# Optimization experiments

Measured on AMD Instinct MI355X. Metric: run time of the kernel, lower is better.

Reference implementation:

```python
import jax, jax.numpy as jnp
import numpy as np


def setup_inputs() -> dict:
    key = jax.random.key(0)
    ks = jax.random.split(key, 8)
    N, E, D, MAX_NODES, C = 100000, 1536, 128, 250000, 2
    embeddings = jax.random.normal(ks[0], (N, E), dtype=jnp.float32)
    node_ids = jnp.arange(N, dtype=jnp.int64)  # default global_ids path
    # persistent node memory buffer (warm state mid-sequence)
    memory = jax.random.normal(ks[1], (MAX_NODES, D), dtype=jnp.float32) * 0.1
    s_ih = 1.0 / np.sqrt(E)
    s_hh = 1.0 / np.sqrt(D)
    w_ih = jax.random.normal(ks[2], (3 * D, E), dtype=jnp.float32) * s_ih
    w_hh = jax.random.normal(ks[3], (3 * D, D), dtype=jnp.float32) * s_hh
    b_ih = jax.random.normal(ks[4], (3 * D,), dtype=jnp.float32) * s_hh
    b_hh = jax.random.normal(ks[5], (3 * D,), dtype=jnp.float32) * s_hh
    s_c = 1.0 / np.sqrt(E + D)
    cls_w = jax.random.normal(ks[6], (C, E + D), dtype=jnp.float32) * s_c
    cls_b = jax.random.normal(ks[7], (C,), dtype=jnp.float32) * s_c
    return {"embeddings": embeddings, "node_ids": node_ids, "memory": memory,
            "w_ih": w_ih, "w_hh": w_hh, "b_ih": b_ih, "b_hh": b_hh,
            "cls_w": cls_w, "cls_b": cls_b}


def reference(embeddings, node_ids, memory, w_ih, w_hh, b_ih, b_hh, cls_w, cls_b):
    # gather previous memory rows for the active nodes: [N, D]
    prev = memory[node_ids]
    # torch.nn.GRUCell math
    gi = embeddings @ w_ih.T + b_ih  # [N, 3D]
    gh = prev @ w_hh.T + b_hh        # [N, 3D]
    i_r, i_z, i_n = jnp.split(gi, 3, axis=1)
    h_r, h_z, h_n = jnp.split(gh, 3, axis=1)
    r = jax.nn.sigmoid(i_r + h_r)
    z = jax.nn.sigmoid(i_z + h_z)
    n = jnp.tanh(i_n + r * h_n)
    new_mem = (1.0 - z) * n + z * prev  # [N, D]
    # scatter updated rows back into the persistent buffer (detached in torch)
    updated_memory = memory.at[node_ids].set(jax.lax.stop_gradient(new_mem))
    # classifier on [embeddings ; new_mem]; dropout is identity in eval
    combined = jnp.concatenate([embeddings, new_mem], axis=1)
    logits = combined @ cls_w.T + cls_b  # [N, 2]
    return logits, updated_memory
```

## Files before the change

### kernel.cpp

```cpp
#include <hip/hip_runtime.h>
#include <hip/hip_bf16.h>

typedef __bf16 bf16;
typedef __bf16 bf16x4 __attribute__((ext_vector_type(4)));
typedef __bf16 bf16x8 __attribute__((ext_vector_type(8)));
typedef float  f32x4  __attribute__((ext_vector_type(4)));

#define EDIM 1536
#define DDIM 128
#define CDIM 1664
#define TM   64
#define NCH  48

#define MFMA_B16(a, b, c) __builtin_amdgcn_mfma_f32_16x16x32_bf16((a), (b), (c), 0, 0, 0)

__device__ __forceinline__ float sigf(float x) { return 1.0f / (1.0f + __expf(-x)); }
__device__ __forceinline__ float tanhf_fast(float x) { return 2.0f / (1.0f + __expf(-2.0f * x)) - 1.0f; }

__device__ __forceinline__ void glds16(const void* g, void* l) {
  __builtin_amdgcn_global_load_lds(
      (const __attribute__((address_space(1))) unsigned int*)g,
      (__attribute__((address_space(3))) unsigned int*)l, 16, 0, 0);
}

template <int LDA>
__device__ __forceinline__ void stageW(const bf16* __restrict__ w, int k0,
                                       char* dst, int wave, int lane) {
#pragma unroll
  for (int j = 0; j < 3; ++j) {
    const int segbase = j * 512 + wave * 64;
    const int seg = segbase + lane;
    const int n = seg >> 2;
    const int q = seg & 3;
    glds16(w + (size_t)n * LDA + k0 + q * 8, dst + (size_t)segbase * 16);
  }
}

__global__ __launch_bounds__(256) void prep_convert(const float* __restrict__ w_ih,
                                                    const float* __restrict__ w_hh,
                                                    bf16* __restrict__ wib,
                                                    bf16* __restrict__ whb) {
  const int i = (blockIdx.x * 256 + threadIdx.x) * 4;
  const int TIH = 3 * DDIM * EDIM;
  const int THH = 3 * DDIM * DDIM;
  if (i < TIH) {
    const float4 v = *(const float4*)(w_ih + i);
    bf16x4 o = {(bf16)v.x, (bf16)v.y, (bf16)v.z, (bf16)v.w};
    *(bf16x4*)(wib + i) = o;
  } else if (i < TIH + THH) {
    const int j = i - TIH;
    const float4 v = *(const float4*)(w_hh + j);
    bf16x4 o = {(bf16)v.x, (bf16)v.y, (bf16)v.z, (bf16)v.w};
    *(bf16x4*)(whb + j) = o;
  }
}

__global__ __launch_bounds__(512, 4) void gru_fused(
    const float* __restrict__ emb, const int* __restrict__ ids,
    const float* __restrict__ mem,
    const float* __restrict__ b_ih, const float* __restrict__ b_hh,
    const float* __restrict__ cls_w, const float* __restrict__ cls_b,
    const bf16* __restrict__ wib, const bf16* __restrict__ whb,
    float* __restrict__ logits, float* __restrict__ omem, int Nrows)
{
  __shared__ char  sW[2][24576];
  __shared__ char  sA[2][5120];
  __shared__ char  sP[16384];
  __shared__ float sLp[64][2];
  __shared__ int   sIds[64];

  const int t    = threadIdx.x;
  const int lane = t & 63;
  const int wave = t >> 6;
  const int wm   = wave >> 2;
  const int wn   = wave & 3;
  const int l15  = lane & 15;
  const int lq   = lane >> 4;
  const int m0   = blockIdx.x * TM;

  if (t < 64)  sIds[t] = (m0 + t < Nrows) ? ids[m0 + t] : 0;
  if (t < 128) sLp[t >> 1][t & 1] = cls_b[t & 1];

  f32x4 accR[2][2], accZ[2][2], accN[2][2], accH[2][2];
#pragma unroll
  for (int sub = 0; sub < 2; ++sub) {
    const int nc = wn * 32 + sub * 16 + l15;
    const float br = b_ih[nc] + b_hh[nc];
    const float bz = b_ih[128 + nc] + b_hh[128 + nc];
    const float bn = b_ih[256 + nc];
    const float bh = b_hh[256 + nc];
#pragma unroll
    for (int mt = 0; mt < 2; ++mt) {
      accR[mt][sub] = (f32x4){br, br, br, br};
      accZ[mt][sub] = (f32x4){bz, bz, bz, bz};
      accN[mt][sub] = (f32x4){bn, bn, bn, bn};
      accH[mt][sub] = (f32x4){bh, bh, bh, bh};
    }
  }

  const int  ar = t >> 3;
  const int  aq = t & 7;
  const bool av = (m0 + ar) < Nrows;
  const float* pA = emb + (size_t)(m0 + ar) * EDIM + aq * 4;
  const int  awofs = ar * 80 + aq * 8;
  float lp0 = 0.f, lp1 = 0.f;

  stageW<EDIM>(wib, 0, sW[0], wave, lane);
  {
    float4 a = make_float4(0.f, 0.f, 0.f, 0.f);
    if (av) a = *(const float4*)pA;
    const float4 c0 = *(const float4*)(cls_w + aq * 4);
    const float4 c1 = *(const float4*)(cls_w + CDIM + aq * 4);
    lp0 += a.x * c0.x + a.y * c0.y + a.z * c0.z + a.w * c0.w;
    lp1 += a.x * c1.x + a.y * c1.y + a.z * c1.z + a.w * c1.w;
    bf16x4 o = {(bf16)a.x, (bf16)a.y, (bf16)a.z, (bf16)a.w};
    *(bf16x4*)(sA[0] + awofs) = o;
  }
  __syncthreads();

  for (int s = 0; s < NCH; ++s) {
    const int cur = s & 1, nxt = cur ^ 1;
    const bool pf = (s + 1) < NCH;
    if (pf) stageW<EDIM>(wib, (s + 1) * 32, sW[nxt], wave, lane);

    bf16x8 af[2];
#pragma unroll
    for (int mt = 0; mt < 2; ++mt) {
      const int m = wm * 32 + mt * 16 + l15;
      af[mt] = *(bf16x8*)(sA[cur] + m * 80 + lq * 16);
    }
#pragma unroll
    for (int g = 0; g < 3; ++g) {
#pragma unroll
      for (int sub = 0; sub < 2; ++sub) {
        const int n = g * 128 + wn * 32 + sub * 16 + l15;
        const bf16x8 bfr = *(bf16x8*)(sW[cur] + n * 64 + lq * 16);
        if (g == 0) {
          accR[0][sub] = MFMA_B16(af[0], bfr, accR[0][sub]);
          accR[1][sub] = MFMA_B16(af[1], bfr, accR[1][sub]);
        } else if (g == 1) {
          accZ[0][sub] = MFMA_B16(af[0], bfr, accZ[0][sub]);
          accZ[1][sub] = MFMA_B16(af[1], bfr, accZ[1][sub]);
        } else {
          accN[0][sub] = MFMA_B16(af[0], bfr, accN[0][sub]);
          accN[1][sub] = MFMA_B16(af[1], bfr, accN[1][sub]);
        }
      }
    }
    if (pf) {
      const int kn = (s + 1) * 32;
      float4 a = make_float4(0.f, 0.f, 0.f, 0.f);
      if (av) a = *(const float4*)(pA + kn);
      const float4 c0 = *(const float4*)(cls_w + kn + aq * 4);
      const float4 c1 = *(const float4*)(cls_w + CDIM + kn + aq * 4);
      lp0 += a.x * c0.x + a.y * c0.y + a.z * c0.z + a.w * c0.w;
      lp1 += a.x * c1.x + a.y * c1.y + a.z * c1.z + a.w * c1.w;
      bf16x4 o = {(bf16)a.x, (bf16)a.y, (bf16)a.z, (bf16)a.w};
      *(bf16x4*)(sA[nxt] + awofs) = o;
    }
    __syncthreads();
  }

  {
    float v0 = lp0, v1 = lp1;
    v0 += __shfl_xor(v0, 1); v0 += __shfl_xor(v0, 2); v0 += __shfl_xor(v0, 4);
    v1 += __shfl_xor(v1, 1); v1 += __shfl_xor(v1, 2); v1 += __shfl_xor(v1, 4);
    if ((lane & 7) == 0) {
      atomicAdd(&sLp[ar][0], v0);
      atomicAdd(&sLp[ar][1], v1);
    }
  }

  stageW<DDIM>(whb, 0, sW[0], wave, lane);
  {
    const int prow = t >> 5;
    const int pc   = t & 31;
#pragma unroll
    for (int p = 0; p < 4; ++p) {
      const int r = p * 16 + prow;
      const float4 v = *(const float4*)(mem + (size_t)sIds[r] * DDIM + pc * 4);
      bf16x4 o = {(bf16)v.x, (bf16)v.y, (bf16)v.z, (bf16)v.w};
      *(bf16x4*)(sP + r * 256 + ((pc << 3) ^ ((r & 7) << 4))) = o;
    }
  }
  __syncthreads();

  for (int ks = 0; ks < 4; ++ks) {
    const int cur = ks & 1, nxt = cur ^ 1;
    if (ks + 1 < 4) stageW<DDIM>(whb, (ks + 1) * 32, sW[nxt], wave, lane);
    bf16x8 af[2];
#pragma unroll
    for (int mt = 0; mt < 2; ++mt) {
      const int m = wm * 32 + mt * 16 + l15;
      const int kb = (ks * 32 + lq * 8) << 1;
      af[mt] = *(bf16x8*)(sP + m * 256 + (kb ^ ((m & 7) << 4)));
    }
#pragma unroll
    for (int g = 0; g < 3; ++g) {
#pragma unroll
      for (int sub = 0; sub < 2; ++sub) {
        const int n = g * 128 + wn * 32 + sub * 16 + l15;
        const bf16x8 bfr = *(bf16x8*)(sW[cur] + n * 64 + lq * 16);
        if (g == 0) {
          accR[0][sub] = MFMA_B16(af[0], bfr, accR[0][sub]);
          accR[1][sub] = MFMA_B16(af[1], bfr, accR[1][sub]);
        } else if (g == 1) {
          accZ[0][sub] = MFMA_B16(af[0], bfr, accZ[0][sub]);
          accZ[1][sub] = MFMA_B16(af[1], bfr, accZ[1][sub]);
        } else {
          accH[0][sub] = MFMA_B16(af[0], bfr, accH[0][sub]);
          accH[1][sub] = MFMA_B16(af[1], bfr, accH[1][sub]);
        }
      }
    }
    __syncthreads();
  }

  float lpM[8][2];
#pragma unroll
  for (int i = 0; i < 8; ++i) { lpM[i][0] = 0.f; lpM[i][1] = 0.f; }

#pragma unroll
  for (int mt = 0; mt < 2; ++mt) {
#pragma unroll
    for (int sub = 0; sub < 2; ++sub) {
      const int d = wn * 32 + sub * 16 + l15;
      const float cw0 = cls_w[EDIM + d];
      const float cw1 = cls_w[CDIM + EDIM + d];
#pragma unroll
      for (int j = 0; j < 4; ++j) {
        const int m = wm * 32 + mt * 16 + lq * 4 + j;
        const float r = sigf(accR[mt][sub][j]);
        const float z = sigf(accZ[mt][sub][j]);
        const float n = tanhf_fast(accN[mt][sub][j] + r * accH[mt][sub][j]);
        const float pv = mem[(size_t)sIds[m] * DDIM + d];
        const float nv = (1.0f - z) * n + z * pv;
        if (m0 + m < Nrows) omem[(size_t)sIds[m] * DDIM + d] = nv;
        lpM[mt * 4 + j][0] += nv * cw0;
        lpM[mt * 4 + j][1] += nv * cw1;
      }
    }
  }

#pragma unroll
  for (int i = 0; i < 8; ++i) {
#pragma unroll
    for (int c = 0; c < 2; ++c) {
      float v = lpM[i][c];
      v += __shfl_xor(v, 1); v += __shfl_xor(v, 2);
      v += __shfl_xor(v, 4); v += __shfl_xor(v, 8);
      if (l15 == 0) {
        const int m = wm * 32 + (i >> 2) * 16 + lq * 4 + (i & 3);
        atomicAdd(&sLp[m][c], v);
      }
    }
  }
  __syncthreads();

  if (t < 128) {
    const int m = t >> 1, c = t & 1;
    if (m0 + m < Nrows) logits[(size_t)(m0 + m) * 2 + c] = sLp[m][c];
  }
}

extern "C" void kernel_launch(void* const* d_in, const int* in_sizes, int n_in,
                              void* d_out, int out_size, void* d_ws, size_t ws_size,
                              hipStream_t stream) {
  const float* emb   = (const float*)d_in[0];
  const int*   ids   = (const int*)d_in[1];
  const float* mem   = (const float*)d_in[2];
  const float* w_ih  = (const float*)d_in[3];
  const float* w_hh  = (const float*)d_in[4];
  const float* b_ih  = (const float*)d_in[5];
  const float* b_hh  = (const float*)d_in[6];
  const float* cls_w = (const float*)d_in[7];
  const float* cls_b = (const float*)d_in[8];

  const int N    = in_sizes[0] / EDIM;
  const int MAXN = in_sizes[2] / DDIM;

  float* logits = (float*)d_out;
  float* omem   = (float*)d_out + (size_t)N * 2;
  bf16*  wib    = (bf16*)d_ws;
  bf16*  whb    = wib + 3 * DDIM * EDIM;

  hipMemcpyAsync(omem, mem, (size_t)MAXN * DDIM * sizeof(float),
                 hipMemcpyDeviceToDevice, stream);
  const int prep_threads = (3 * DDIM * EDIM + 3 * DDIM * DDIM) / 4;
  prep_convert<<<(prep_threads + 255) / 256, 256, 0, stream>>>(w_ih, w_hh, wib, whb);
  gru_fused<<<(N + TM - 1) / TM, 512, 0, stream>>>(emb, ids, mem, b_ih, b_hh,
                                                   cls_w, cls_b, wib, whb,
                                                   logits, omem, N);
}
```

Measured before the change: 421.5 us.

## Load GRU weight fragments directly into registers and halve row tile

Weight tiles no longer go through shared memory. Each wave now loads its bf16 weight fragments straight from global memory into registers, double-buffered across K steps through an unrolled two-stage macro. The row tile shrinks from 64 to 32 and the block from 512 to 256 threads, so there are twice as many blocks and less shared memory per block. This removes the LDS staging traffic and the shared-memory footprint, but each block now rereads the full weight matrix from global/L2 for only 32 rows, which doubles total weight traffic and adds register pressure.

```diff
diff --git a/kernel.cpp b/kernel.cpp
--- a/kernel.cpp
+++ b/kernel.cpp
@@ -9,32 +9,13 @@
 #define EDIM 1536
 #define DDIM 128
 #define CDIM 1664
-#define TM   64
-#define NCH  48
+#define TM   32
+#define NSTG 48
 
 #define MFMA_B16(a, b, c) __builtin_amdgcn_mfma_f32_16x16x32_bf16((a), (b), (c), 0, 0, 0)
 
 __device__ __forceinline__ float sigf(float x) { return 1.0f / (1.0f + __expf(-x)); }
 __device__ __forceinline__ float tanhf_fast(float x) { return 2.0f / (1.0f + __expf(-2.0f * x)) - 1.0f; }
-
-__device__ __forceinline__ void glds16(const void* g, void* l) {
-  __builtin_amdgcn_global_load_lds(
-      (const __attribute__((address_space(1))) unsigned int*)g,
-      (__attribute__((address_space(3))) unsigned int*)l, 16, 0, 0);
-}
-
-template <int LDA>
-__device__ __forceinline__ void stageW(const bf16* __restrict__ w, int k0,
-                                       char* dst, int wave, int lane) {
-#pragma unroll
-  for (int j = 0; j < 3; ++j) {
-    const int segbase = j * 512 + wave * 64;
-    const int seg = segbase + lane;
-    const int n = seg >> 2;
-    const int q = seg & 3;
-    glds16(w + (size_t)n * LDA + k0 + q * 8, dst + (size_t)segbase * 16);
-  }
-}
 
 __global__ __launch_bounds__(256) void prep_convert(const float* __restrict__ w_ih,
                                                     const float* __restrict__ w_hh,
@@ -55,7 +36,7 @@
   }
 }
 
-__global__ __launch_bounds__(512, 4) void gru_fused(
+__global__ __launch_bounds__(256, 2) void gru_fused(
     const float* __restrict__ emb, const int* __restrict__ ids,
     const float* __restrict__ mem,
     const float* __restrict__ b_ih, const float* __restrict__ b_hh,
@@ -63,23 +44,20 @@
     const bf16* __restrict__ wib, const bf16* __restrict__ whb,
     float* __restrict__ logits, float* __restrict__ omem, int Nrows)
 {
-  __shared__ char  sW[2][24576];
-  __shared__ char  sA[2][5120];
-  __shared__ char  sP[16384];
-  __shared__ float sLp[64][2];
-  __shared__ int   sIds[64];
+  __shared__ char  sA[2][2560];
+  __shared__ char  sP[8192];
+  __shared__ float sLp[32][2];
+  __shared__ int   sIds[32];
 
   const int t    = threadIdx.x;
   const int lane = t & 63;
-  const int wave = t >> 6;
-  const int wm   = wave >> 2;
-  const int wn   = wave & 3;
+  const int wn   = t >> 6;
   const int l15  = lane & 15;
   const int lq   = lane >> 4;
   const int m0   = blockIdx.x * TM;
 
-  if (t < 64)  sIds[t] = (m0 + t < Nrows) ? ids[m0 + t] : 0;
-  if (t < 128) sLp[t >> 1][t & 1] = cls_b[t & 1];
+  if (t < 32) sIds[t] = (m0 + t < Nrows) ? ids[m0 + t] : 0;
+  if (t < 64) sLp[t >> 1][t & 1] = cls_b[t & 1];
 
   f32x4 accR[2][2], accZ[2][2], accN[2][2], accH[2][2];
 #pragma unroll
@@ -105,7 +83,52 @@
   const int  awofs = ar * 80 + aq * 8;
   float lp0 = 0.f, lp1 = 0.f;
 
-  stageW<EDIM>(wib, 0, sW[0], wave, lane);
+  const bf16* pW = wib + (size_t)(wn * 32 + l15) * EDIM + lq * 8;
+
+  bf16x8 wP[6], wQ[6];
+
+#define LOADW(DST, S) do {                                    \
+    const bf16* _p = pW + (size_t)(S) * 32;                   \
+    DST[0] = *(const bf16x8*)(_p);                            \
+    DST[1] = *(const bf16x8*)(_p +  16 * EDIM);               \
+    DST[2] = *(const bf16x8*)(_p + 128 * EDIM);               \
+    DST[3] = *(const bf16x8*)(_p + 144 * EDIM);               \
+    DST[4] = *(const bf16x8*)(_p + 256 * EDIM);               \
+    DST[5] = *(const bf16x8*)(_p + 272 * EDIM);               \
+  } while (0)
+
+#define BODY(S, CUR, WC, WNX, PF) do {                                        \
+    float4 a = make_float4(0.f, 0.f, 0.f, 0.f), c0 = a, c1 = a;               \
+    if (PF) {                                                                 \
+      LOADW(WNX, (S) + 1);                                                    \
+      if (av) a = *(const float4*)(pA + ((S) + 1) * 32);                      \
+      c0 = *(const float4*)(cls_w + ((S) + 1) * 32 + aq * 4);                 \
+      c1 = *(const float4*)(cls_w + CDIM + ((S) + 1) * 32 + aq * 4);          \
+    }                                                                         \
+    bf16x8 af0 = *(bf16x8*)(sA[CUR] + (l15) * 80 + lq * 16);                  \
+    bf16x8 af1 = *(bf16x8*)(sA[CUR] + (16 + l15) * 80 + lq * 16);             \
+    accR[0][0] = MFMA_B16(af0, WC[0], accR[0][0]);                            \
+    accR[1][0] = MFMA_B16(af1, WC[0], accR[1][0]);                            \
+    accR[0][1] = MFMA_B16(af0, WC[1], accR[0][1]);                            \
+    accR[1][1] = MFMA_B16(af1, WC[1], accR[1][1]);                            \
+    accZ[0][0] = MFMA_B16(af0, WC[2], accZ[0][0]);                            \
+    accZ[1][0] = MFMA_B16(af1, WC[2], accZ[1][0]);                            \
+    accZ[0][1] = MFMA_B16(af0, WC[3], accZ[0][1]);                            \
+    accZ[1][1] = MFMA_B16(af1, WC[3], accZ[1][1]);                            \
+    accN[0][0] = MFMA_B16(af0, WC[4], accN[0][0]);                            \
+    accN[1][0] = MFMA_B16(af1, WC[4], accN[1][0]);                            \
+    accN[0][1] = MFMA_B16(af0, WC[5], accN[0][1]);                            \
+    accN[1][1] = MFMA_B16(af1, WC[5], accN[1][1]);                            \
+    if (PF) {                                                                 \
+      lp0 += a.x * c0.x + a.y * c0.y + a.z * c0.z + a.w * c0.w;               \
+      lp1 += a.x * c1.x + a.y * c1.y + a.z * c1.z + a.w * c1.w;               \
+      bf16x4 o = {(bf16)a.x, (bf16)a.y, (bf16)a.z, (bf16)a.w};                \
+      *(bf16x4*)(sA[(CUR) ^ 1] + awofs) = o;                                  \
+    }                                                                         \
+    __syncthreads();                                                          \
+  } while (0)
+
+  LOADW(wP, 0);
   {
     float4 a = make_float4(0.f, 0.f, 0.f, 0.f);
     if (av) a = *(const float4*)pA;
@@ -118,47 +141,9 @@
   }
   __syncthreads();
 
-  for (int s = 0; s < NCH; ++s) {
-    const int cur = s & 1, nxt = cur ^ 1;
-    const bool pf = (s + 1) < NCH;
-    if (pf) stageW<EDIM>(wib, (s + 1) * 32, sW[nxt], wave, lane);
-
-    bf16x8 af[2];
-#pragma unroll
-    for (int mt = 0; mt < 2; ++mt) {
-      const int m = wm * 32 + mt * 16 + l15;
-      af[mt] = *(bf16x8*)(sA[cur] + m * 80 + lq * 16);
-    }
-#pragma unroll
-    for (int g = 0; g < 3; ++g) {
-#pragma unroll
-      for (int sub = 0; sub < 2; ++sub) {
-        const int n = g * 128 + wn * 32 + sub * 16 + l15;
-        const bf16x8 bfr = *(bf16x8*)(sW[cur] + n * 64 + lq * 16);
-        if (g == 0) {
-          accR[0][sub] = MFMA_B16(af[0], bfr, accR[0][sub]);
-          accR[1][sub] = MFMA_B16(af[1], bfr, accR[1][sub]);
-        } else if (g == 1) {
-          accZ[0][sub] = MFMA_B16(af[0], bfr, accZ[0][sub]);
-          accZ[1][sub] = MFMA_B16(af[1], bfr, accZ[1][sub]);
-        } else {
-          accN[0][sub] = MFMA_B16(af[0], bfr, accN[0][sub]);
-          accN[1][sub] = MFMA_B16(af[1], bfr, accN[1][sub]);
-        }
-      }
-    }
-    if (pf) {
-      const int kn = (s + 1) * 32;
-      float4 a = make_float4(0.f, 0.f, 0.f, 0.f);
-      if (av) a = *(const float4*)(pA + kn);
-      const float4 c0 = *(const float4*)(cls_w + kn + aq * 4);
-      const float4 c1 = *(const float4*)(cls_w + CDIM + kn + aq * 4);
-      lp0 += a.x * c0.x + a.y * c0.y + a.z * c0.z + a.w * c0.w;
-      lp1 += a.x * c1.x + a.y * c1.y + a.z * c1.z + a.w * c1.w;
-      bf16x4 o = {(bf16)a.x, (bf16)a.y, (bf16)a.z, (bf16)a.w};
-      *(bf16x4*)(sA[nxt] + awofs) = o;
-    }
-    __syncthreads();
+  for (int s = 0; s < NSTG; s += 2) {
+    BODY(s, 0, wP, wQ, true);
+    BODY(s + 1, 1, wQ, wP, (s + 2) < NSTG);
   }
 
   {
@@ -171,13 +156,12 @@
     }
   }
 
-  stageW<DDIM>(whb, 0, sW[0], wave, lane);
   {
     const int prow = t >> 5;
     const int pc   = t & 31;
 #pragma unroll
     for (int p = 0; p < 4; ++p) {
-      const int r = p * 16 + prow;
+      const int r = p * 8 + prow;
       const float4 v = *(const float4*)(mem + (size_t)sIds[r] * DDIM + pc * 4);
       bf16x4 o = {(bf16)v.x, (bf16)v.y, (bf16)v.z, (bf16)v.w};
       *(bf16x4*)(sP + r * 256 + ((pc << 3) ^ ((r & 7) << 4))) = o;
@@ -185,22 +169,22 @@
   }
   __syncthreads();
 
+#pragma unroll
   for (int ks = 0; ks < 4; ++ks) {
-    const int cur = ks & 1, nxt = cur ^ 1;
-    if (ks + 1 < 4) stageW<DDIM>(whb, (ks + 1) * 32, sW[nxt], wave, lane);
     bf16x8 af[2];
 #pragma unroll
     for (int mt = 0; mt < 2; ++mt) {
-      const int m = wm * 32 + mt * 16 + l15;
+      const int m = mt * 16 + l15;
       const int kb = (ks * 32 + lq * 8) << 1;
       af[mt] = *(bf16x8*)(sP + m * 256 + (kb ^ ((m & 7) << 4)));
     }
+    const int kg = ks * 32 + lq * 8;
 #pragma unroll
     for (int g = 0; g < 3; ++g) {
 #pragma unroll
       for (int sub = 0; sub < 2; ++sub) {
         const int n = g * 128 + wn * 32 + sub * 16 + l15;
-        const bf16x8 bfr = *(bf16x8*)(sW[cur] + n * 64 + lq * 16);
+        const bf16x8 bfr = *(const bf16x8*)(whb + n * DDIM + kg);
         if (g == 0) {
           accR[0][sub] = MFMA_B16(af[0], bfr, accR[0][sub]);
           accR[1][sub] = MFMA_B16(af[1], bfr, accR[1][sub]);
@@ -213,7 +197,6 @@
         }
       }
     }
-    __syncthreads();
   }
 
   float lpM[8][2];
@@ -229,7 +212,7 @@
       const float cw1 = cls_w[CDIM + EDIM + d];
 #pragma unroll
       for (int j = 0; j < 4; ++j) {
-        const int m = wm * 32 + mt * 16 + lq * 4 + j;
+        const int m = mt * 16 + lq * 4 + j;
         const float r = sigf(accR[mt][sub][j]);
         const float z = sigf(accZ[mt][sub][j]);
         const float n = tanhf_fast(accN[mt][sub][j] + r * accH[mt][sub][j]);
@@ -250,14 +233,14 @@
       v += __shfl_xor(v, 1); v += __shfl_xor(v, 2);
       v += __shfl_xor(v, 4); v += __shfl_xor(v, 8);
       if (l15 == 0) {
-        const int m = wm * 32 + (i >> 2) * 16 + lq * 4 + (i & 3);
+        const int m = (i >> 2) * 16 + lq * 4 + (i & 3);
         atomicAdd(&sLp[m][c], v);
       }
     }
   }
   __syncthreads();
 
-  if (t < 128) {
+  if (t < 64) {
     const int m = t >> 1, c = t & 1;
     if (m0 + m < Nrows) logits[(size_t)(m0 + m) * 2 + c] = sLp[m][c];
   }
@@ -288,7 +271,7 @@
                  hipMemcpyDeviceToDevice, stream);
   const int prep_threads = (3 * DDIM * EDIM + 3 * DDIM * DDIM) / 4;
   prep_convert<<<(prep_threads + 255) / 256, 256, 0, stream>>>(w_ih, w_hh, wib, whb);
-  gru_fused<<<(N + TM - 1) / TM, 512, 0, stream>>>(emb, ids, mem, b_ih, b_hh,
+  gru_fused<<<(N + TM - 1) / TM, 256, 0, stream>>>(emb, ids, mem, b_ih, b_hh,
                                                    cls_w, cls_b, wib, whb,
                                                    logits, omem, N);
 }
```

Result: slower. 660.7 us (+56.8%).

## Compute classifier logits via MFMA and prefetch embeddings several chunks ahead

Applied to the files above, without the earlier changes.

The per-thread scalar FMA dot product of embeddings with cls_w is replaced. cls_w is converted to bf16 once into shared memory, and the classifier becomes an extra MFMA per chunk on wave column 0, reusing the A fragments already loaded. The main K loop is unrolled by four, with register-held embedding loads issued several chunks early to hide global latency. This reduces the cls_w global loads and VALU work, at the cost of more registers and bf16 precision on the embedding part of the classifier.

```diff
diff --git a/kernel.cpp b/kernel.cpp
--- a/kernel.cpp
+++ b/kernel.cpp
@@ -29,9 +29,9 @@
 #pragma unroll
   for (int j = 0; j < 3; ++j) {
     const int segbase = j * 512 + wave * 64;
-    const int seg = segbase + lane;
-    const int n = seg >> 2;
-    const int q = seg & 3;
+    const int s = segbase + lane;
+    const int n = s >> 2;
+    const int q = s & 3;
     glds16(w + (size_t)n * LDA + k0 + q * 8, dst + (size_t)segbase * 16);
   }
 }
@@ -65,7 +65,7 @@
 {
   __shared__ char  sW[2][24576];
   __shared__ char  sA[2][5120];
-  __shared__ char  sP[16384];
+  __shared__ char  sPC[16384];
   __shared__ float sLp[64][2];
   __shared__ int   sIds[64];
 
@@ -81,7 +81,7 @@
   if (t < 64)  sIds[t] = (m0 + t < Nrows) ? ids[m0 + t] : 0;
   if (t < 128) sLp[t >> 1][t & 1] = cls_b[t & 1];
 
-  f32x4 accR[2][2], accZ[2][2], accN[2][2], accH[2][2];
+  f32x4 accR[2][2], accZ[2][2], accN[2][2], accH[2][2], accC[2];
 #pragma unroll
   for (int sub = 0; sub < 2; ++sub) {
     const int nc = wn * 32 + sub * 16 + l15;
@@ -97,79 +97,93 @@
       accH[mt][sub] = (f32x4){bh, bh, bh, bh};
     }
   }
+  accC[0] = (f32x4){0.f, 0.f, 0.f, 0.f};
+  accC[1] = (f32x4){0.f, 0.f, 0.f, 0.f};
 
   const int  ar = t >> 3;
   const int  aq = t & 7;
   const bool av = (m0 + ar) < Nrows;
   const float* pA = emb + (size_t)(m0 + ar) * EDIM + aq * 4;
   const int  awofs = ar * 80 + aq * 8;
-  float lp0 = 0.f, lp1 = 0.f;
+  const float4 fz = make_float4(0.f, 0.f, 0.f, 0.f);
+  float4 aA = fz, aB = fz, aC = fz, aD = fz;
 
   stageW<EDIM>(wib, 0, sW[0], wave, lane);
+  if (t < 384) {
+    const int i = t * 8;
+    const int r = (i >= 1536) ? 1 : 0;
+    const int col = i - r * 1536;
+    const float4 u0 = *(const float4*)(cls_w + r * CDIM + col);
+    const float4 u1 = *(const float4*)(cls_w + r * CDIM + col + 4);
+    bf16x8 o = {(bf16)u0.x, (bf16)u0.y, (bf16)u0.z, (bf16)u0.w,
+                (bf16)u1.x, (bf16)u1.y, (bf16)u1.z, (bf16)u1.w};
+    *(bf16x8*)(sPC + t * 16) = o;
+  }
   {
-    float4 a = make_float4(0.f, 0.f, 0.f, 0.f);
-    if (av) a = *(const float4*)pA;
-    const float4 c0 = *(const float4*)(cls_w + aq * 4);
-    const float4 c1 = *(const float4*)(cls_w + CDIM + aq * 4);
-    lp0 += a.x * c0.x + a.y * c0.y + a.z * c0.z + a.w * c0.w;
-    lp1 += a.x * c1.x + a.y * c1.y + a.z * c1.z + a.w * c1.w;
+    float4 a = av ? *(const float4*)pA : fz;
     bf16x4 o = {(bf16)a.x, (bf16)a.y, (bf16)a.z, (bf16)a.w};
     *(bf16x4*)(sA[0] + awofs) = o;
+    if (av) {
+      aA = *(const float4*)(pA + 32);
+      aB = *(const float4*)(pA + 64);
+      aC = *(const float4*)(pA + 96);
+    }
   }
   __syncthreads();
 
-  for (int s = 0; s < NCH; ++s) {
-    const int cur = s & 1, nxt = cur ^ 1;
-    const bool pf = (s + 1) < NCH;
-    if (pf) stageW<EDIM>(wib, (s + 1) * 32, sW[nxt], wave, lane);
-
-    bf16x8 af[2];
-#pragma unroll
-    for (int mt = 0; mt < 2; ++mt) {
-      const int m = wm * 32 + mt * 16 + l15;
-      af[mt] = *(bf16x8*)(sA[cur] + m * 80 + lq * 16);
-    }
-#pragma unroll
-    for (int g = 0; g < 3; ++g) {
-#pragma unroll
-      for (int sub = 0; sub < 2; ++sub) {
-        const int n = g * 128 + wn * 32 + sub * 16 + l15;
-        const bf16x8 bfr = *(bf16x8*)(sW[cur] + n * 64 + lq * 16);
-        if (g == 0) {
-          accR[0][sub] = MFMA_B16(af[0], bfr, accR[0][sub]);
-          accR[1][sub] = MFMA_B16(af[1], bfr, accR[1][sub]);
-        } else if (g == 1) {
-          accZ[0][sub] = MFMA_B16(af[0], bfr, accZ[0][sub]);
-          accZ[1][sub] = MFMA_B16(af[1], bfr, accZ[1][sub]);
-        } else {
-          accN[0][sub] = MFMA_B16(af[0], bfr, accN[0][sub]);
-          accN[1][sub] = MFMA_B16(af[1], bfr, accN[1][sub]);
-        }
-      }
-    }
-    if (pf) {
-      const int kn = (s + 1) * 32;
-      float4 a = make_float4(0.f, 0.f, 0.f, 0.f);
-      if (av) a = *(const float4*)(pA + kn);
-      const float4 c0 = *(const float4*)(cls_w + kn + aq * 4);
-      const float4 c1 = *(const float4*)(cls_w + CDIM + kn + aq * 4);
-      lp0 += a.x * c0.x + a.y * c0.y + a.z * c0.z + a.w * c0.w;
-      lp1 += a.x * c1.x + a.y * c1.y + a.z * c1.z + a.w * c1.w;
-      bf16x4 o = {(bf16)a.x, (bf16)a.y, (bf16)a.z, (bf16)a.w};
-      *(bf16x4*)(sA[nxt] + awofs) = o;
-    }
-    __syncthreads();
-  }
-
-  {
-    float v0 = lp0, v1 = lp1;
-    v0 += __shfl_xor(v0, 1); v0 += __shfl_xor(v0, 2); v0 += __shfl_xor(v0, 4);
-    v1 += __shfl_xor(v1, 1); v1 += __shfl_xor(v1, 2); v1 += __shfl_xor(v1, 4);
-    if ((lane & 7) == 0) {
-      atomicAdd(&sLp[ar][0], v0);
-      atomicAdd(&sLp[ar][1], v1);
-    }
-  }
+#define BODY(C, AREG) do {                                                     \
+    const int cur_ = (C) & 1, nxt_ = cur_ ^ 1;                                 \
+    const bool pf_ = (C) + 1 < NCH;                                            \
+    if (pf_) stageW<EDIM>(wib, ((C) + 1) * 32, sW[nxt_], wave, lane);          \
+    bf16x8 af0_ = *(bf16x8*)(sA[cur_] + (wm * 32 + l15) * 80 + lq * 16);       \
+    bf16x8 af1_ = *(bf16x8*)(sA[cur_] + (wm * 32 + 16 + l15) * 80 + lq * 16);  \
+    _Pragma("unroll")                                                          \
+    for (int g_ = 0; g_ < 3; ++g_) {                                           \
+      _Pragma("unroll")                                                        \
+      for (int sub_ = 0; sub_ < 2; ++sub_) {                                   \
+        const int n_ = g_ * 128 + wn * 32 + sub_ * 16 + l15;                   \
+        const bf16x8 bfr_ = *(bf16x8*)(sW[cur_] + n_ * 64 + lq * 16);          \
+        if (g_ == 0) {                                                         \
+          accR[0][sub_] = MFMA_B16(af0_, bfr_, accR[0][sub_]);                 \
+          accR[1][sub_] = MFMA_B16(af1_, bfr_, accR[1][sub_]);                 \
+        } else if (g_ == 1) {                                                  \
+          accZ[0][sub_] = MFMA_B16(af0_, bfr_, accZ[0][sub_]);                 \
+          accZ[1][sub_] = MFMA_B16(af1_, bfr_, accZ[1][sub_]);                 \
+        } else {                                                               \
+          accN[0][sub_] = MFMA_B16(af0_, bfr_, accN[0][sub_]);                 \
+          accN[1][sub_] = MFMA_B16(af1_, bfr_, accN[1][sub_]);                 \
+        }                                                                      \
+      }                                                                        \
+    }                                                                          \
+    if (wn == 0) {       \
+      bf16x8 bc_ = {(bf16)0.f, (bf16)0.f, (bf16)0.f, (bf16)0.f,                \
+                    (bf16)0.f, (bf16)0.f, (bf16)0.f, (bf16)0.f};               \
+      if (l15 < 2) bc_ = *(bf16x8*)(sPC + l15 * 3072 + (C) * 64 + lq * 16);    \
+      accC[0] = MFMA_B16(af0_, bc_, accC[0]);                                  \
+      accC[1] = MFMA_B16(af1_, bc_, accC[1]);                                  \
+    }                                                                          \
+    if (pf_) {                                                                 \
+      bf16x4 o_ = {(bf16)(AREG).x, (bf16)(AREG).y,                             \
+                   (bf16)(AREG).z, (bf16)(AREG).w};                            \
+      *(bf16x4*)(sA[nxt_] + awofs) = o_;                                       \
+    }                                                                          \
+    __syncthreads();                                                           \
+  } while (0)
+
+  for (int S = 0; S < 12; ++S) {
+    const int c0 = S * 4;
+    if (S < 11 && av) aD = *(const float4*)(pA + (c0 + 4) * 32);
+    BODY(c0,     aA);
+    BODY(c0 + 1, aB);
+    BODY(c0 + 2, aC);
+    if (S < 11 && av) {
+      aA = *(const float4*)(pA + (c0 + 5) * 32);
+      aB = *(const float4*)(pA + (c0 + 6) * 32);
+      aC = *(const float4*)(pA + (c0 + 7) * 32);
+    }
+    BODY(c0 + 3, aD);
+  }
+#undef BODY
 
   stageW<DDIM>(whb, 0, sW[0], wave, lane);
   {
@@ -180,7 +194,7 @@
       const int r = p * 16 + prow;
       const float4 v = *(const float4*)(mem + (size_t)sIds[r] * DDIM + pc * 4);
       bf16x4 o = {(bf16)v.x, (bf16)v.y, (bf16)v.z, (bf16)v.w};
-      *(bf16x4*)(sP + r * 256 + ((pc << 3) ^ ((r & 7) << 4))) = o;
+      *(bf16x4*)(sPC + r * 256 + ((pc << 3) ^ ((r & 7) << 4))) = o;
     }
   }
   __syncthreads();
@@ -193,7 +207,7 @@
     for (int mt = 0; mt < 2; ++mt) {
       const int m = wm * 32 + mt * 16 + l15;
       const int kb = (ks * 32 + lq * 8) << 1;
-      af[mt] = *(bf16x8*)(sP + m * 256 + (kb ^ ((m & 7) << 4)));
+      af[mt] = *(bf16x8*)(sPC + m * 256 + (kb ^ ((m & 7) << 4)));
     }
 #pragma unroll
     for (int g = 0; g < 3; ++g) {
@@ -242,6 +256,14 @@
     }
   }
 
+  if (wn == 0 && l15 < 2) {
+#pragma unroll
+    for (int mt = 0; mt < 2; ++mt)
+#pragma unroll
+      for (int j = 0; j < 4; ++j)
+        atomicAdd(&sLp[wm * 32 + mt * 16 + lq * 4 + j][l15], accC[mt][j]);
+  }
+
 #pragma unroll
   for (int i = 0; i < 8; ++i) {
 #pragma unroll
```

Result: slower. 465.8 us (+10.5%).
